# Performance work log

Measured on AMD Instinct MI355X. Metric: run time of the kernel, lower is better.

Reference implementation:

```python
import jax, jax.numpy as jnp
import numpy as np

B, N, M, DQ, DK, DV, H = 8, 1024, 1024, 512, 512, 512, 8
DS = DV // H  # dim_split = 64
NEG = -1e38


def _ln(x, g, b, eps=1e-5):
    mu = jnp.mean(x, -1, keepdims=True)
    var = jnp.mean((x - mu) ** 2, -1, keepdims=True)
    return (x - mu) * jax.lax.rsqrt(var + eps) * g + b


def setup_inputs() -> dict:
    key = jax.random.key(0)
    ks = jax.random.split(key, 16)
    s = 0.02
    return {
        "x": jax.random.normal(ks[0], (B, N, DQ), jnp.float32),
        "y": jax.random.normal(ks[1], (B, M, DK), jnp.float32),
        "x_mask": jax.random.randint(ks[2], (B, N), 0, 2).astype(bool),
        "y_mask": jax.random.randint(ks[3], (B, M), 0, 2).astype(bool),
        "Wq": jax.random.normal(ks[4], (DQ, DV), jnp.float32) * s,
        "Wk": jax.random.normal(ks[5], (DK, DV), jnp.float32) * s,
        "Wv": jax.random.normal(ks[6], (DK, DV), jnp.float32) * s,
        "Wo": jax.random.normal(ks[7], (DV, DQ), jnp.float32) * s,
        "W1": jax.random.normal(ks[8], (DQ, DQ), jnp.float32) * s,
        "b1": jnp.zeros((DQ,), jnp.float32),
        "W2": jax.random.normal(ks[9], (DQ, DQ), jnp.float32) * s,
        "b2": jnp.zeros((DQ,), jnp.float32),
        "g1": jnp.ones((DQ,), jnp.float32),
        "be1": jnp.zeros((DQ,), jnp.float32),
        "g2": jnp.ones((DQ,), jnp.float32),
        "be2": jnp.zeros((DQ,), jnp.float32),
    }


def reference(x, y, x_mask, y_mask, Wq, Wk, Wv, Wo, W1, b1, W2, b2, g1, be1, g2, be2):
    xm = x_mask[..., None]  # [B,N,1]
    ym = y_mask[..., None]  # [B,M,1]
    x = jnp.where(xm, 0.0, x)
    y = jnp.where(ym, 0.0, y)
    # projections (no bias); masked rows stay zero, re-mask as in source
    q = jnp.where(xm, 0.0, x @ Wq).reshape(B, N, H, DS)
    k = jnp.where(ym, 0.0, y @ Wk).reshape(B, M, H, DS)
    v = jnp.where(ym, 0.0, y @ Wv).reshape(B, M, H, DS)
    # scaled dot product; NOTE: scale is sqrt(dim_v), faithful to source
    sdp = jnp.einsum('bnhd,bmhd->bhnm', q, k) / np.sqrt(DV)
    mask = x_mask[:, None, :, None] | y_mask[:, None, None, :]  # [B,1,N,M]
    sdp = jnp.where(mask, NEG, sdp)
    alpha = jax.nn.softmax(sdp, axis=-1)  # softmax over keys (slot_att=False)
    att = jnp.einsum('bhnm,bmhd->bnhd', alpha, v).reshape(B, N, DV)
    att = jnp.where(xm, 0.0, att)
    o = x + att @ Wo
    o = _ln(o, g1, be1)
    ff = jax.nn.relu(o @ W1 + b1) @ W2 + b2
    o = _ln(o + ff, g2, be2)
    return jnp.where(xm, 0.0, o)
```

## Files before the change

kernel.cpp:

```cpp
#include <hip/hip_runtime.h>
#include <hip/hip_bf16.h>

typedef __bf16 bf16;
typedef __attribute__((ext_vector_type(4))) __bf16 bf16x4;
typedef __attribute__((ext_vector_type(8))) __bf16 bf16x8;
typedef __attribute__((ext_vector_type(4))) float f32x4;

#define B_ 8
#define N_ 1024
#define M_ 1024
#define H_ 8
#define ROWS_ (B_ * N_)

__device__ __forceinline__ f32x4 mfma16(bf16x8 a, bf16x8 b, f32x4 c) {
    return __builtin_amdgcn_mfma_f32_16x16x32_bf16(a, b, c, 0, 0, 0);
}

__device__ __forceinline__ void glds16(const void* g, void* l) {
    __builtin_amdgcn_global_load_lds((const __attribute__((address_space(1))) void*)g,
                                     (__attribute__((address_space(3))) void*)l, 16, 0, 0);
}

__global__ __launch_bounds__(256) void prep(const float* __restrict__ x, const float* __restrict__ y,
                                            bf16* __restrict__ Xb, bf16* __restrict__ Yb,
                                            const float* W0, const float* W1, const float* W2,
                                            const float* W3, const float* W4, const float* W5,
                                            bf16* T0, bf16* T1, bf16* T2, bf16* T3, bf16* T4, bf16* T5) {
    __shared__ float t[64][65];
    int bid = blockIdx.x;
    if (bid < 8192) {
        int i = bid * 256 + threadIdx.x;
        const float4* s;
        bf16x4* d;
        int j;
        if (i < 1048576) { s = (const float4*)x; d = (bf16x4*)Xb; j = i; }
        else             { s = (const float4*)y; d = (bf16x4*)Yb; j = i - 1048576; }
        float4 f = s[j];
        bf16x4 o = {(bf16)f.x, (bf16)f.y, (bf16)f.z, (bf16)f.w};
        d[j] = o;
        return;
    }
    int wb = bid - 8192;
    const float* srcs[6] = {W0, W1, W2, W3, W4, W5};
    bf16* dsts[6] = {T0, T1, T2, T3, T4, T5};
    const float* W = srcs[wb >> 6];
    bf16* Wt = dsts[wb >> 6];
    int tile = wb & 63;
    int k0 = (tile >> 3) * 64, n0 = (tile & 7) * 64;
    int tx = threadIdx.x & 63, ty = threadIdx.x >> 6;
#pragma unroll
    for (int j = 0; j < 16; ++j)
        t[ty + j * 4][tx] = W[(size_t)(k0 + ty + j * 4) * 512 + n0 + tx];
    __syncthreads();
#pragma unroll
    for (int j = 0; j < 16; ++j)
        Wt[(size_t)(n0 + ty + j * 4) * 512 + k0 + tx] = (bf16)t[tx][ty + j * 4];
}

__device__ __forceinline__ void gemm_core(const bf16* __restrict__ A, const bf16* __restrict__ Bt,
                                          int row0, int col0, char* AsB, char* BsB, f32x4 acc[2][4]) {
    int tid = threadIdx.x, wave = tid >> 6, lane = tid & 63;
    int lr = lane & 15, q4 = lane >> 4;
    const bf16 *Asrc[4], *Bsrc[2];
#pragma unroll
    for (int s = 0; s < 4; ++s) {
        int c = tid + s * 256, r = c >> 3, bk = (c & 7) ^ (r & 7);
        Asrc[s] = A + (size_t)(row0 + r) * 512 + bk * 8;
    }
#pragma unroll
    for (int s = 0; s < 2; ++s) {
        int c = tid + s * 256, r = c >> 3, bk = (c & 7) ^ (r & 7);
        Bsrc[s] = Bt + (size_t)(col0 + r) * 512 + bk * 8;
    }
    int wb = wave * 1024;
#pragma unroll
    for (int s = 0; s < 4; ++s) glds16(Asrc[s], AsB + s * 4096 + wb);
#pragma unroll
    for (int s = 0; s < 2; ++s) glds16(Bsrc[s], BsB + s * 4096 + wb);
#pragma unroll
    for (int it = 0; it < 8; ++it) {
        __syncthreads();
        const char* Ac = AsB + (it & 1) * 16384;
        const char* Bc = BsB + (it & 1) * 8192;
        if (it < 7) {
            char* An = AsB + ((it + 1) & 1) * 16384;
            char* Bn = BsB + ((it + 1) & 1) * 8192;
            int k0 = (it + 1) * 64;
#pragma unroll
            for (int s = 0; s < 4; ++s) glds16(Asrc[s] + k0, An + s * 4096 + wb);
#pragma unroll
            for (int s = 0; s < 2; ++s) glds16(Bsrc[s] + k0, Bn + s * 4096 + wb);
        }
        bf16x8 af[2][2], bfr[4][2];
#pragma unroll
        for (int rt = 0; rt < 2; ++rt) {
            int row = wave * 32 + rt * 16 + lr;
#pragma unroll
            for (int c = 0; c < 2; ++c)
                af[rt][c] = *(const bf16x8*)(Ac + (row * 8 + ((c * 4 + q4) ^ (row & 7))) * 16);
        }
#pragma unroll
        for (int ct = 0; ct < 4; ++ct) {
            int col = ct * 16 + lr;
#pragma unroll
            for (int c = 0; c < 2; ++c)
                bfr[ct][c] = *(const bf16x8*)(Bc + (col * 8 + ((c * 4 + q4) ^ (col & 7))) * 16);
        }
#pragma unroll
        for (int rt = 0; rt < 2; ++rt)
#pragma unroll
            for (int ct = 0; ct < 4; ++ct) {
                acc[rt][ct] = mfma16(af[rt][0], bfr[ct][0], acc[rt][ct]);
                acc[rt][ct] = mfma16(af[rt][1], bfr[ct][1], acc[rt][ct]);
            }
    }
}

__global__ __launch_bounds__(256, 2) void proj_qkv(const bf16* __restrict__ Xb, const bf16* __restrict__ Yb,
                                                   const bf16* __restrict__ Wqt, const bf16* __restrict__ Wkt,
                                                   const bf16* __restrict__ Wvt,
                                                   bf16* __restrict__ qb, bf16* __restrict__ kb,
                                                   bf16* __restrict__ Vt) {
    __shared__ char AsB[2 * 16384];
    __shared__ char BsB[2 * 8192];
    int z = blockIdx.z;
    const bf16 *A, *Bt;
    int row0, col0;
    if (z == 0)      { A = Xb;  Bt = Wqt; row0 = blockIdx.x * 128; col0 = blockIdx.y * 64; }
    else if (z == 1) { A = Yb;  Bt = Wkt; row0 = blockIdx.x * 128; col0 = blockIdx.y * 64; }
    else { A = Wvt; Bt = Yb; int flat = blockIdx.y * 64 + blockIdx.x; row0 = (flat & 3) * 128; col0 = (flat >> 2) * 64; }
    const f32x4 z4 = {0.f, 0.f, 0.f, 0.f};
    f32x4 acc[2][4] = {{z4, z4, z4, z4}, {z4, z4, z4, z4}};
    gemm_core(A, Bt, row0, col0, AsB, BsB, acc);
    int wave = threadIdx.x >> 6, lane = threadIdx.x & 63, lr = lane & 15, q4 = lane >> 4;
    bf16* dst = (z == 0) ? qb : kb;
    const float cl = 0.06376373228f;
    float sc = (z == 0) ? cl : 1.0f;
#pragma unroll
    for (int rt = 0; rt < 2; ++rt)
#pragma unroll
        for (int ct = 0; ct < 4; ++ct) {
            int col = col0 + ct * 16 + lr;
#pragma unroll
            for (int r = 0; r < 4; ++r) {
                int row = row0 + wave * 32 + rt * 16 + q4 * 4 + r;
                bf16 v = (bf16)(acc[rt][ct][r] * sc);
                if (z < 2) dst[(size_t)row * 512 + col] = v;
                else Vt[(size_t)((col >> 10) * 512 + row) * 1024 + (col & 1023)] = v;
            }
        }
}

template <int BIAS, int RELU>
__global__ __launch_bounds__(256, 2) void gemm_bt(const bf16* __restrict__ A, const bf16* __restrict__ Bt,
                                                  const float* __restrict__ bias, bf16* __restrict__ Cout) {
    __shared__ char AsB[2 * 16384];
    __shared__ char BsB[2 * 8192];
    int row0 = blockIdx.x * 128, col0 = blockIdx.y * 64;
    const f32x4 z4 = {0.f, 0.f, 0.f, 0.f};
    f32x4 acc[2][4] = {{z4, z4, z4, z4}, {z4, z4, z4, z4}};
    gemm_core(A, Bt, row0, col0, AsB, BsB, acc);
    int wave = threadIdx.x >> 6, lane = threadIdx.x & 63, lr = lane & 15, q4 = lane >> 4;
#pragma unroll
    for (int rt = 0; rt < 2; ++rt)
#pragma unroll
        for (int ct = 0; ct < 4; ++ct) {
            int col = col0 + ct * 16 + lr;
            float bv = BIAS ? bias[col] : 0.0f;
#pragma unroll
            for (int r = 0; r < 4; ++r) {
                int row = row0 + wave * 32 + rt * 16 + q4 * 4 + r;
                float v = acc[rt][ct][r] + bv;
                if (RELU) v = fmaxf(v, 0.0f);
                Cout[(size_t)row * 512 + col] = (bf16)v;
            }
        }
}

__global__ __launch_bounds__(512, 2) void attn(const bf16* __restrict__ Q, const bf16* __restrict__ Kb,
                                               const bf16* __restrict__ Vt, const int* __restrict__ ymask,
                                               bf16* __restrict__ att) {
    __shared__ bf16 Ks[2][64 * 64];
    __shared__ bf16 Vs[2][64 * 64];
    __shared__ bf16 Ps[8][16 * 72];
    __shared__ float fmk[1024];

    int bid = blockIdx.x;
    int bh = bid & 63, n0 = (bid >> 6) * 128;
    int b = bh >> 3, h = bh & 7;
    int tid = threadIdx.x, wave = tid >> 6, lane = tid & 63;
    int lr = lane & 15, q4 = lane >> 4;

    const int* ymb = ymask + (b << 10);
    fmk[tid]       = ymb[tid]       ? -1e38f : 0.0f;
    fmk[tid + 512] = ymb[tid + 512] ? -1e38f : 0.0f;

    const bf16* qp = Q + (size_t)((b << 10) + n0 + wave * 16 + lr) * 512 + h * 64 + q4 * 8;
    bf16x8 aq0 = *(const bf16x8*)qp;
    bf16x8 aq1 = *(const bf16x8*)(qp + 32);

    bf16 one1 = (bf16)1.0f;
    bf16x8 ones = {one1, one1, one1, one1, one1, one1, one1, one1};

    int r = tid >> 3, bk = (tid & 7) ^ (r & 7);
    const bf16* Ksrc = Kb + (size_t)((b << 10) + r) * 512 + h * 64 + bk * 8;
    const bf16* Vsrc = Vt + (size_t)(b * 512 + h * 64 + r) * 1024 + bk * 8;
    int ldso = tid * 16;

    const f32x4 zv = {0.f, 0.f, 0.f, 0.f};
    f32x4 O[4] = {zv, zv, zv, zv};
    f32x4 O4 = zv;

    glds16(Ksrc, (char*)Ks[0] + ldso);
    glds16(Vsrc, (char*)Vs[0] + ldso);

    for (int it = 0; it < 16; ++it) {
        __syncthreads();
        const char* K_ = (const char*)Ks[it & 1];
        const char* V_ = (const char*)Vs[it & 1];
        if (it < 15) {
            size_t m1 = (size_t)(it + 1) * 64;
            glds16(Ksrc + m1 * 512, (char*)Ks[(it + 1) & 1] + ldso);
            glds16(Vsrc + m1, (char*)Vs[(it + 1) & 1] + ldso);
        }

#pragma unroll
        for (int nt = 0; nt < 4; ++nt) {
            int krow = nt * 16 + lr;
            bf16x8 kf0 = *(const bf16x8*)(K_ + (krow * 8 + (q4 ^ (krow & 7))) * 16);
            bf16x8 kf1 = *(const bf16x8*)(K_ + (krow * 8 + ((4 + q4) ^ (krow & 7))) * 16);
            float fm = fmk[it * 64 + krow];
            f32x4 s = {fm, fm, fm, fm};
            s = mfma16(aq0, kf0, s);
            s = mfma16(aq1, kf1, s);
#pragma unroll
            for (int rr = 0; rr < 4; ++rr)
                Ps[wave][(q4 * 4 + rr) * 72 + krow] = (bf16)exp2f(s[rr]);
        }
        bf16x8 ap0 = *(const bf16x8*)&Ps[wave][lr * 72 + q4 * 8];
        bf16x8 ap1 = *(const bf16x8*)&Ps[wave][lr * 72 + 32 + q4 * 8];
        O4 = mfma16(ap0, ones, O4);
        O4 = mfma16(ap1, ones, O4);
#pragma unroll
        for (int dt = 0; dt < 4; ++dt) {
            int vrow = dt * 16 + lr;
            bf16x8 vf0 = *(const bf16x8*)(V_ + (vrow * 8 + (q4 ^ (vrow & 7))) * 16);
            bf16x8 vf1 = *(const bf16x8*)(V_ + (vrow * 8 + ((4 + q4) ^ (vrow & 7))) * 16);
            O[dt] = mfma16(ap0, vf0, O[dt]);
            O[dt] = mfma16(ap1, vf1, O[dt]);
        }
    }

    float inv[4];
#pragma unroll
    for (int rr = 0; rr < 4; ++rr)
        inv[rr] = (O4[rr] > 0.0f) ? (1.0f / O4[rr]) : 0.0f;
#pragma unroll
    for (int dt = 0; dt < 4; ++dt)
#pragma unroll
        for (int rr = 0; rr < 4; ++rr) {
            int row = n0 + wave * 16 + q4 * 4 + rr;
            att[(size_t)((b << 10) + row) * 512 + h * 64 + dt * 16 + lr] =
                (bf16)(O[dt][rr] * inv[rr]);
        }
}

__global__ __launch_bounds__(128) void ln1_k(const float* __restrict__ X, const bf16* __restrict__ A,
                                             const float* __restrict__ g, const float* __restrict__ be,
                                             bf16* __restrict__ Obf) {
    int row = blockIdx.x, t = threadIdx.x;
    float4 xv = ((const float4*)(X + (size_t)row * 512))[t];
    bf16x4 av = ((const bf16x4*)(A + (size_t)row * 512))[t];
    float4 o = {xv.x + (float)av.x, xv.y + (float)av.y, xv.z + (float)av.z, xv.w + (float)av.w};
    float s = o.x + o.y + o.z + o.w;
    float sq = o.x * o.x + o.y * o.y + o.z * o.z + o.w * o.w;
#pragma unroll
    for (int off = 1; off < 64; off <<= 1) { s += __shfl_xor(s, off); sq += __shfl_xor(sq, off); }
    __shared__ float ls[2], lq[2];
    if ((t & 63) == 0) { ls[t >> 6] = s; lq[t >> 6] = sq; }
    __syncthreads();
    s = ls[0] + ls[1]; sq = lq[0] + lq[1];
    float mu = s * (1.0f / 512.0f);
    float var = sq * (1.0f / 512.0f) - mu * mu;
    float rs = rsqrtf(var + 1e-5f);
    float4 gv = ((const float4*)g)[t];
    float4 bv = ((const float4*)be)[t];
    bf16x4 b4 = {(bf16)((o.x - mu) * rs * gv.x + bv.x), (bf16)((o.y - mu) * rs * gv.y + bv.y),
                 (bf16)((o.z - mu) * rs * gv.z + bv.z), (bf16)((o.w - mu) * rs * gv.w + bv.w)};
    ((bf16x4*)(Obf + (size_t)row * 512))[t] = b4;
}

__global__ __launch_bounds__(128) void ln2_k(const bf16* __restrict__ Ob, const bf16* __restrict__ F,
                                             const float* __restrict__ g, const float* __restrict__ be,
                                             const int* __restrict__ xmask, float* __restrict__ out) {
    int row = blockIdx.x, t = threadIdx.x;
    bf16x4 xv = ((const bf16x4*)(Ob + (size_t)row * 512))[t];
    bf16x4 rv = ((const bf16x4*)(F + (size_t)row * 512))[t];
    float4 o = {(float)xv.x + (float)rv.x, (float)xv.y + (float)rv.y,
                (float)xv.z + (float)rv.z, (float)xv.w + (float)rv.w};
    float s = o.x + o.y + o.z + o.w;
    float sq = o.x * o.x + o.y * o.y + o.z * o.z + o.w * o.w;
#pragma unroll
    for (int off = 1; off < 64; off <<= 1) { s += __shfl_xor(s, off); sq += __shfl_xor(sq, off); }
    __shared__ float ls[2], lq[2];
    if ((t & 63) == 0) { ls[t >> 6] = s; lq[t >> 6] = sq; }
    __syncthreads();
    s = ls[0] + ls[1]; sq = lq[0] + lq[1];
    float mu = s * (1.0f / 512.0f);
    float var = sq * (1.0f / 512.0f) - mu * mu;
    float rs = rsqrtf(var + 1e-5f);
    int msk = xmask[row];
    float4 gv = ((const float4*)g)[t];
    float4 bv = ((const float4*)be)[t];
    float4 r4 = {(o.x - mu) * rs * gv.x + bv.x, (o.y - mu) * rs * gv.y + bv.y,
                 (o.z - mu) * rs * gv.z + bv.z, (o.w - mu) * rs * gv.w + bv.w};
    if (msk) r4 = {0.f, 0.f, 0.f, 0.f};
    ((float4*)(out + (size_t)row * 512))[t] = r4;
}

extern "C" void kernel_launch(void* const* d_in, const int* in_sizes, int n_in,
                              void* d_out, int out_size, void* d_ws, size_t ws_size,
                              hipStream_t stream) {
    const float* x   = (const float*)d_in[0];
    const float* y   = (const float*)d_in[1];
    const int*   xm  = (const int*)d_in[2];
    const int*   ym  = (const int*)d_in[3];
    const float* Wq  = (const float*)d_in[4];
    const float* Wk  = (const float*)d_in[5];
    const float* Wv  = (const float*)d_in[6];
    const float* Wo  = (const float*)d_in[7];
    const float* W1  = (const float*)d_in[8];
    const float* b1  = (const float*)d_in[9];
    const float* W2  = (const float*)d_in[10];
    const float* b2  = (const float*)d_in[11];
    const float* g1  = (const float*)d_in[12];
    const float* be1 = (const float*)d_in[13];
    const float* g2  = (const float*)d_in[14];
    const float* be2 = (const float*)d_in[15];

    char* ws = (char*)d_ws;
    const size_t WT_SZ  = 512 * 512 * sizeof(bf16);
    const size_t XB_SZ  = (size_t)ROWS_ * 512 * sizeof(bf16);

    bf16* Wqt = (bf16*)(ws + 0 * WT_SZ);
    bf16* Wkt = (bf16*)(ws + 1 * WT_SZ);
    bf16* Wvt = (bf16*)(ws + 2 * WT_SZ);
    bf16* Wot = (bf16*)(ws + 3 * WT_SZ);
    bf16* W1t = (bf16*)(ws + 4 * WT_SZ);
    bf16* W2t = (bf16*)(ws + 5 * WT_SZ);
    size_t off = 6 * WT_SZ;
    bf16* Xb  = (bf16*)(ws + off); off += XB_SZ;
    bf16* Yb  = (bf16*)(ws + off); off += XB_SZ;
    bf16* qb  = (bf16*)(ws + off); off += XB_SZ;
    bf16* kb  = (bf16*)(ws + off); off += XB_SZ;
    bf16* Vt  = (bf16*)(ws + off); off += XB_SZ;
    bf16* attb = Xb;
    bf16* awo  = kb;
    bf16* obf  = qb;
    bf16* hb   = Yb;
    bf16* fb   = Vt;

    prep<<<8576, 256, 0, stream>>>(x, y, Xb, Yb, Wq, Wk, Wv, Wo, W1, W2,
                                   Wqt, Wkt, Wvt, Wot, W1t, W2t);

    proj_qkv<<<dim3(64, 8, 3), 256, 0, stream>>>(Xb, Yb, Wqt, Wkt, Wvt, qb, kb, Vt);

    attn<<<512, 512, 0, stream>>>(qb, kb, Vt, ym, attb);

    dim3 gg(64, 8);
    gemm_bt<0, 0><<<gg, 256, 0, stream>>>(attb, Wot, nullptr, awo);
    ln1_k<<<ROWS_, 128, 0, stream>>>(x, awo, g1, be1, obf);
    gemm_bt<1, 1><<<gg, 256, 0, stream>>>(obf, W1t, b1, hb);
    gemm_bt<1, 0><<<gg, 256, 0, stream>>>(hb, W2t, b2, fb);
    ln2_k<<<ROWS_, 128, 0, stream>>>(obf, fb, g2, be2, xm, (float*)d_out);
}
```

Baseline: 217.9 us.

## Enlarge GEMM tiles to 128x128 with eight waves per block

```diff
diff --git a/kernel.cpp b/kernel.cpp
--- a/kernel.cpp
+++ b/kernel.cpp
@@ -61,47 +61,46 @@
                                           int row0, int col0, char* AsB, char* BsB, f32x4 acc[2][4]) {
     int tid = threadIdx.x, wave = tid >> 6, lane = tid & 63;
     int lr = lane & 15, q4 = lane >> 4;
-    const bf16 *Asrc[4], *Bsrc[2];
-#pragma unroll
-    for (int s = 0; s < 4; ++s) {
-        int c = tid + s * 256, r = c >> 3, bk = (c & 7) ^ (r & 7);
+    int rbase = (wave & 3) * 32, cbase = (wave >> 2) * 64;
+    const bf16 *Asrc[2], *Bsrc[2];
+#pragma unroll
+    for (int s = 0; s < 2; ++s) {
+        int c = tid + s * 512, r = c >> 3, bk = (c & 7) ^ (r & 7);
         Asrc[s] = A + (size_t)(row0 + r) * 512 + bk * 8;
-    }
+        Bsrc[s] = Bt + (size_t)(col0 + r) * 512 + bk * 8;
+    }
+    int wb = wave * 1024;
 #pragma unroll
     for (int s = 0; s < 2; ++s) {
-        int c = tid + s * 256, r = c >> 3, bk = (c & 7) ^ (r & 7);
-        Bsrc[s] = Bt + (size_t)(col0 + r) * 512 + bk * 8;
-    }
-    int wb = wave * 1024;
-#pragma unroll
-    for (int s = 0; s < 4; ++s) glds16(Asrc[s], AsB + s * 4096 + wb);
-#pragma unroll
-    for (int s = 0; s < 2; ++s) glds16(Bsrc[s], BsB + s * 4096 + wb);
+        glds16(Asrc[s], AsB + s * 8192 + wb);
+        glds16(Bsrc[s], BsB + s * 8192 + wb);
+    }
 #pragma unroll
     for (int it = 0; it < 8; ++it) {
         __syncthreads();
         const char* Ac = AsB + (it & 1) * 16384;
-        const char* Bc = BsB + (it & 1) * 8192;
+        const char* Bc = BsB + (it & 1) * 16384;
         if (it < 7) {
             char* An = AsB + ((it + 1) & 1) * 16384;
-            char* Bn = BsB + ((it + 1) & 1) * 8192;
+            char* Bn = BsB + ((it + 1) & 1) * 16384;
             int k0 = (it + 1) * 64;
 #pragma unroll
-            for (int s = 0; s < 4; ++s) glds16(Asrc[s] + k0, An + s * 4096 + wb);
-#pragma unroll
-            for (int s = 0; s < 2; ++s) glds16(Bsrc[s] + k0, Bn + s * 4096 + wb);
+            for (int s = 0; s < 2; ++s) {
+                glds16(Asrc[s] + k0, An + s * 8192 + wb);
+                glds16(Bsrc[s] + k0, Bn + s * 8192 + wb);
+            }
         }
         bf16x8 af[2][2], bfr[4][2];
 #pragma unroll
         for (int rt = 0; rt < 2; ++rt) {
-            int row = wave * 32 + rt * 16 + lr;
+            int row = rbase + rt * 16 + lr;
 #pragma unroll
             for (int c = 0; c < 2; ++c)
                 af[rt][c] = *(const bf16x8*)(Ac + (row * 8 + ((c * 4 + q4) ^ (row & 7))) * 16);
         }
 #pragma unroll
         for (int ct = 0; ct < 4; ++ct) {
-            int col = ct * 16 + lr;
+            int col = cbase + ct * 16 + lr;
 #pragma unroll
             for (int c = 0; c < 2; ++c)
                 bfr[ct][c] = *(const bf16x8*)(Bc + (col * 8 + ((c * 4 + q4) ^ (col & 7))) * 16);
@@ -116,23 +115,24 @@
     }
 }
 
-__global__ __launch_bounds__(256, 2) void proj_qkv(const bf16* __restrict__ Xb, const bf16* __restrict__ Yb,
+__global__ __launch_bounds__(512, 2) void proj_qkv(const bf16* __restrict__ Xb, const bf16* __restrict__ Yb,
                                                    const bf16* __restrict__ Wqt, const bf16* __restrict__ Wkt,
                                                    const bf16* __restrict__ Wvt,
                                                    bf16* __restrict__ qb, bf16* __restrict__ kb,
                                                    bf16* __restrict__ Vt) {
     __shared__ char AsB[2 * 16384];
-    __shared__ char BsB[2 * 8192];
+    __shared__ char BsB[2 * 16384];
     int z = blockIdx.z;
     const bf16 *A, *Bt;
     int row0, col0;
-    if (z == 0)      { A = Xb;  Bt = Wqt; row0 = blockIdx.x * 128; col0 = blockIdx.y * 64; }
-    else if (z == 1) { A = Yb;  Bt = Wkt; row0 = blockIdx.x * 128; col0 = blockIdx.y * 64; }
-    else { A = Wvt; Bt = Yb; int flat = blockIdx.y * 64 + blockIdx.x; row0 = (flat & 3) * 128; col0 = (flat >> 2) * 64; }
+    if (z == 0)      { A = Xb;  Bt = Wqt; row0 = blockIdx.x * 128; col0 = blockIdx.y * 128; }
+    else if (z == 1) { A = Yb;  Bt = Wkt; row0 = blockIdx.x * 128; col0 = blockIdx.y * 128; }
+    else             { A = Wvt; Bt = Yb;  row0 = blockIdx.y * 128; col0 = blockIdx.x * 128; }
     const f32x4 z4 = {0.f, 0.f, 0.f, 0.f};
     f32x4 acc[2][4] = {{z4, z4, z4, z4}, {z4, z4, z4, z4}};
     gemm_core(A, Bt, row0, col0, AsB, BsB, acc);
     int wave = threadIdx.x >> 6, lane = threadIdx.x & 63, lr = lane & 15, q4 = lane >> 4;
+    int rbase = (wave & 3) * 32, cbase = (wave >> 2) * 64;
     bf16* dst = (z == 0) ? qb : kb;
     const float cl = 0.06376373228f;
     float sc = (z == 0) ? cl : 1.0f;
@@ -140,10 +140,10 @@
     for (int rt = 0; rt < 2; ++rt)
 #pragma unroll
         for (int ct = 0; ct < 4; ++ct) {
-            int col = col0 + ct * 16 + lr;
+            int col = col0 + cbase + ct * 16 + lr;
 #pragma unroll
             for (int r = 0; r < 4; ++r) {
-                int row = row0 + wave * 32 + rt * 16 + q4 * 4 + r;
+                int row = row0 + rbase + rt * 16 + q4 * 4 + r;
                 bf16 v = (bf16)(acc[rt][ct][r] * sc);
                 if (z < 2) dst[(size_t)row * 512 + col] = v;
                 else Vt[(size_t)((col >> 10) * 512 + row) * 1024 + (col & 1023)] = v;
@@ -152,24 +152,25 @@
 }
 
 template <int BIAS, int RELU>
-__global__ __launch_bounds__(256, 2) void gemm_bt(const bf16* __restrict__ A, const bf16* __restrict__ Bt,
+__global__ __launch_bounds__(512, 2) void gemm_bt(const bf16* __restrict__ A, const bf16* __restrict__ Bt,
                                                   const float* __restrict__ bias, bf16* __restrict__ Cout) {
     __shared__ char AsB[2 * 16384];
-    __shared__ char BsB[2 * 8192];
-    int row0 = blockIdx.x * 128, col0 = blockIdx.y * 64;
+    __shared__ char BsB[2 * 16384];
+    int row0 = blockIdx.x * 128, col0 = blockIdx.y * 128;
     const f32x4 z4 = {0.f, 0.f, 0.f, 0.f};
     f32x4 acc[2][4] = {{z4, z4, z4, z4}, {z4, z4, z4, z4}};
     gemm_core(A, Bt, row0, col0, AsB, BsB, acc);
     int wave = threadIdx.x >> 6, lane = threadIdx.x & 63, lr = lane & 15, q4 = lane >> 4;
+    int rbase = (wave & 3) * 32, cbase = (wave >> 2) * 64;
 #pragma unroll
     for (int rt = 0; rt < 2; ++rt)
 #pragma unroll
         for (int ct = 0; ct < 4; ++ct) {
-            int col = col0 + ct * 16 + lr;
+            int col = col0 + cbase + ct * 16 + lr;
             float bv = BIAS ? bias[col] : 0.0f;
 #pragma unroll
             for (int r = 0; r < 4; ++r) {
-                int row = row0 + wave * 32 + rt * 16 + q4 * 4 + r;
+                int row = row0 + rbase + rt * 16 + q4 * 4 + r;
                 float v = acc[rt][ct][r] + bv;
                 if (RELU) v = fmaxf(v, 0.0f);
                 Cout[(size_t)row * 512 + col] = (bf16)v;
@@ -363,14 +364,14 @@
     prep<<<8576, 256, 0, stream>>>(x, y, Xb, Yb, Wq, Wk, Wv, Wo, W1, W2,
                                    Wqt, Wkt, Wvt, Wot, W1t, W2t);
 
-    proj_qkv<<<dim3(64, 8, 3), 256, 0, stream>>>(Xb, Yb, Wqt, Wkt, Wvt, qb, kb, Vt);
+    proj_qkv<<<dim3(64, 4, 3), 512, 0, stream>>>(Xb, Yb, Wqt, Wkt, Wvt, qb, kb, Vt);
 
     attn<<<512, 512, 0, stream>>>(qb, kb, Vt, ym, attb);
 
-    dim3 gg(64, 8);
-    gemm_bt<0, 0><<<gg, 256, 0, stream>>>(attb, Wot, nullptr, awo);
+    dim3 gg(64, 4);
+    gemm_bt<0, 0><<<gg, 512, 0, stream>>>(attb, Wot, nullptr, awo);
     ln1_k<<<ROWS_, 128, 0, stream>>>(x, awo, g1, be1, obf);
-    gemm_bt<1, 1><<<gg, 256, 0, stream>>>(obf, W1t, b1, hb);
-    gemm_bt<1, 0><<<gg, 256, 0, stream>>>(hb, W2t, b2, fb);
+    gemm_bt<1, 1><<<gg, 512, 0, stream>>>(obf, W1t, b1, hb);
+    gemm_bt<1, 0><<<gg, 512, 0, stream>>>(hb, W2t, b2, fb);
     ln2_k<<<ROWS_, 128, 0, stream>>>(obf, fb, g2, be2, xm, (float*)d_out);
 }
```

Result: faster. 213.1 us (-2.2%).
